# Optimization experiments

Measured on AMD Instinct MI355X. Metric: run time of the kernel, lower is better.

## Reference

```python
import jax, jax.numpy as jnp
import numpy as np

B, S, D, H, MEL = 64, 512, 512, 8, 80
HD = D // H  # head dim


def _lstm_cell(x, h, c, w_ih, w_hh, b_ih, b_hh):
    # torch gate order: i, f, g, o
    gates = x @ w_ih.T + h @ w_hh.T + b_ih + b_hh
    i, f, g, o = jnp.split(gates, 4, axis=-1)
    c = jax.nn.sigmoid(f) * c + jax.nn.sigmoid(i) * jnp.tanh(g)
    h = jax.nn.sigmoid(o) * jnp.tanh(c)
    return h, c


def setup_inputs() -> dict:
    key = jax.random.key(0)
    ks = jax.random.split(key, 24)
    s = 0.05
    inp = {"encoder_output": jax.random.normal(ks[0], (B, S, D), jnp.float32)}
    # MultiheadAttention params (torch layout: in_proj [3D, D])
    inp["attn_in_w"] = jax.random.normal(ks[1], (3 * D, D), jnp.float32) * s
    inp["attn_in_b"] = jax.random.normal(ks[2], (3 * D,), jnp.float32) * s
    inp["attn_out_w"] = jax.random.normal(ks[3], (D, D), jnp.float32) * s
    inp["attn_out_b"] = jax.random.normal(ks[4], (D,), jnp.float32) * s
    # LSTM1 (2 layers)
    names = [("l1_w_ih0", (4 * D, D)), ("l1_w_hh0", (4 * D, D)), ("l1_b_ih0", (4 * D,)), ("l1_b_hh0", (4 * D,)),
             ("l1_w_ih1", (4 * D, D)), ("l1_w_hh1", (4 * D, D)), ("l1_b_ih1", (4 * D,)), ("l1_b_hh1", (4 * D,)),
             ("l2_w_ih", (4 * D, D)), ("l2_w_hh", (4 * D, D)), ("l2_b_ih", (4 * D,)), ("l2_b_hh", (4 * D,)),
             ("proj_w", (MEL, D)), ("proj_b", (MEL,))]
    for i, (n, shp) in enumerate(names):
        inp[n] = jax.random.normal(ks[5 + i], shp, jnp.float32) * s
    return inp


def reference(encoder_output, attn_in_w, attn_in_b, attn_out_w, attn_out_b,
              l1_w_ih0, l1_w_hh0, l1_b_ih0, l1_b_hh0,
              l1_w_ih1, l1_w_hh1, l1_b_ih1, l1_b_hh1,
              l2_w_ih, l2_w_hh, l2_b_ih, l2_b_hh, proj_w, proj_b):
    b, s, d = encoder_output.shape
    max_len = s * 5
    wq, wk, wv = jnp.split(attn_in_w, 3, axis=0)
    bq, bk, bv = jnp.split(attn_in_b, 3, axis=0)
    # Precompute K, V over encoder output: [B, S, H, HD]
    K = (encoder_output @ wk.T + bk).reshape(b, s, H, HD)
    V = (encoder_output @ wv.T + bv).reshape(b, s, H, HD)
    scale = 1.0 / np.sqrt(HD)

    def attend(x):  # x: [B, D] single-token query
        q = ((x @ wq.T + bq) * scale).reshape(b, H, HD)
        scores = jnp.einsum('bhd,bshd->bhs', q, K)
        w = jax.nn.softmax(scores, axis=-1)
        ctx = jnp.einsum('bhs,bshd->bhd', w, V).reshape(b, d)
        return ctx @ attn_out_w.T + attn_out_b

    zeros = jnp.zeros((b, d), encoder_output.dtype)
    carry0 = (zeros, zeros, zeros, zeros, zeros, zeros, zeros)

    def step(carry, _):
        h10, c10, h11, c11, h2, c2, dec_in = carry
        h10, c10 = _lstm_cell(dec_in, h10, c10, l1_w_ih0, l1_w_hh0, l1_b_ih0, l1_b_hh0)
        h11, c11 = _lstm_cell(h10, h11, c11, l1_w_ih1, l1_w_hh1, l1_b_ih1, l1_b_hh1)
        attn_out = attend(h11)
        h2, c2 = _lstm_cell(attn_out, h2, c2, l2_w_ih, l2_w_hh, l2_b_ih, l2_b_hh)
        out = h2 @ proj_w.T + proj_b  # [B, MEL]
        return (h10, c10, h11, c11, h2, c2, h2), out

    _, ys = jax.lax.scan(step, carry0, None, length=max_len)
    return jnp.transpose(ys, (1, 0, 2))  # [B, max_len, MEL]
```

## Files before the change

### kernel.cpp

```cpp
#include <hip/hip_runtime.h>
#include <hip/hip_bf16.h>
#include <hip/hip_fp8.h>

#define DEV_INLINE __device__ __forceinline__

typedef __attribute__((ext_vector_type(8))) short bf16x8;
typedef __attribute__((ext_vector_type(4))) float f32x4;
typedef unsigned long long ull;

constexpr int Bc = 64, Sc = 512, Dc = 512, Hc = 8, HDc = 64, MELc = 80, Tc = 2560;
constexpr int OUTSTRIDE = Tc * MELc;

constexpr size_t SZ_KP8 = 64ull * 8 * 512 * 64;
constexpr size_t SZ_VP  = 64ull * 8 * 512 * 64 * 2;
constexpr size_t SZ_PL  = 128ull * 2048 * 16;
constexpr size_t OFF_KP8 = 0;
constexpr size_t OFF_VP  = OFF_KP8 + SZ_KP8;
constexpr size_t OFF_PL0 = OFF_VP + SZ_VP;
constexpr size_t OFF_PL1 = OFF_PL0 + SZ_PL;
constexpr size_t OFF_PL2 = OFF_PL1 + SZ_PL;
constexpr size_t OFF_PWQ = OFF_PL2 + SZ_PL;
constexpr size_t OFF_PP  = OFF_PWQ + 524288;
constexpr size_t OFF_BL0 = OFF_PP + 81920;
constexpr size_t OFF_BL1 = OFF_BL0 + 8192;
constexpr size_t OFF_BL2 = OFF_BL1 + 8192;
constexpr size_t OFF_B2E = OFF_BL2 + 8192;
constexpr size_t OFF_W2E = OFF_B2E + 8192;
constexpr size_t OFF_WOT = OFF_W2E + 2097152;
constexpr size_t OFF_ACT = OFF_WOT + 1048576;
constexpr size_t OFF_FLG = OFF_ACT + 524288;

constexpr unsigned DYN_LDS = 137344;

DEV_INLINE float bf2f(short s) { return __uint_as_float(((unsigned)(unsigned short)s) << 16); }
DEV_INLINE short f2bf(float f) { union { __hip_bfloat16 h; short s; } u; u.h = __float2bfloat16(f); return u.s; }
DEV_INLINE float sig_f(float x) { return 1.0f / (1.0f + __expf(-x)); }
DEV_INLINE float tanh_f(float x) {
  float ax = fabsf(x);
  float e = __expf(fminf(2.0f * ax, 80.0f));
  float r = 1.0f - 2.0f / (e + 1.0f);
  return copysignf(r, x);
}
DEV_INLINE bf16x8 cvt8(const float* p) {
  bf16x8 r;
#pragma unroll
  for (int i = 0; i < 8; ++i) r[i] = f2bf(p[i]);
  return r;
}
DEV_INLINE float fp8tof(unsigned v) {
  __hip_fp8_e4m3 t; t.__x = (__hip_fp8_storage_t)v; return (float)t;
}

DEV_INLINE ull ld_dev_u64(const void* p) {
  return __hip_atomic_load((const ull*)p, __ATOMIC_RELAXED, __HIP_MEMORY_SCOPE_AGENT);
}
DEV_INLINE void st_dev_u64(void* p, ull v) {
  __hip_atomic_store((ull*)p, v, __ATOMIC_RELAXED, __HIP_MEMORY_SCOPE_AGENT);
}
DEV_INLINE bf16x8 ld_frag(const __hip_bfloat16* p) {
  union { bf16x8 v; ull u[2]; } r;
  r.u[0] = ld_dev_u64(p);
  r.u[1] = ld_dev_u64((const char*)p + 8);
  return r.v;
}

__global__ __launch_bounds__(256) void gemm_setup(const float* __restrict__ A,
                                                  const float* __restrict__ Bt,
                                                  const float* __restrict__ bias,
                                                  __hip_bfloat16* __restrict__ dst,
                                                  unsigned char* __restrict__ dst8,
                                                  int mode) {
  int tid = threadIdx.x, lane = tid & 63, wv = tid >> 6;
  int m0 = blockIdx.y * 64 + wv * 16;
  int nb = blockIdx.x * 64;
  int mrow = m0 + (lane & 15);
  int kb = (lane >> 4) * 8;
  f32x4 acc0 = {0,0,0,0}, acc1 = {0,0,0,0}, acc2 = {0,0,0,0}, acc3 = {0,0,0,0};
  const float* arow = A + (size_t)mrow * 512 + kb;
  const float* b0r = Bt + (size_t)(nb + 0 * 16 + (lane & 15)) * 512 + kb;
  const float* b1r = Bt + (size_t)(nb + 1 * 16 + (lane & 15)) * 512 + kb;
  const float* b2r = Bt + (size_t)(nb + 2 * 16 + (lane & 15)) * 512 + kb;
  const float* b3r = Bt + (size_t)(nb + 3 * 16 + (lane & 15)) * 512 + kb;
  for (int kk = 0; kk < 16; ++kk) {
    bf16x8 af = cvt8(arow + kk * 32);
    acc0 = __builtin_amdgcn_mfma_f32_16x16x32_bf16(af, cvt8(b0r + kk * 32), acc0, 0, 0, 0);
    acc1 = __builtin_amdgcn_mfma_f32_16x16x32_bf16(af, cvt8(b1r + kk * 32), acc1, 0, 0, 0);
    acc2 = __builtin_amdgcn_mfma_f32_16x16x32_bf16(af, cvt8(b2r + kk * 32), acc2, 0, 0, 0);
    acc3 = __builtin_amdgcn_mfma_f32_16x16x32_bf16(af, cvt8(b3r + kk * 32), acc3, 0, 0, 0);
  }
  int col16 = lane & 15, r0 = (lane >> 4) * 4;
  f32x4 accs[4] = {acc0, acc1, acc2, acc3};
#pragma unroll
  for (int nt = 0; nt < 4; ++nt) {
    int n = nb + nt * 16 + col16;
#pragma unroll
    for (int r = 0; r < 4; ++r) {
      int m = m0 + r0 + r;
      float v = accs[nt][r];
      if (mode == 0) {
        v += bias[n];
        int bb = m >> 9, s = m & 511, h = n >> 6, d = n & 63;
        dst[(((size_t)(bb * 8 + h) * 512 + s) * 64) + d] = __float2bfloat16(v);
      } else if (mode == 2) {
        v += bias[n];
        int bb = m >> 9, s = m & 511, h = n >> 6, d = n & 63;
        __hip_fp8_e4m3 q(v);
        dst8[(((size_t)(bb * 8 + h) * 512 + s) * 64) + d] = (unsigned char)q.__x;
      } else {
        dst[(size_t)m * 512 + n] = __float2bfloat16(v);
      }
    }
  }
}

__global__ __launch_bounds__(256) void transpose512(const float* __restrict__ in, float* __restrict__ out) {
  __shared__ float tl[32][33];
  int x = threadIdx.x & 31, ty = threadIdx.x >> 5;
  int bx = blockIdx.x * 32, by = blockIdx.y * 32;
#pragma unroll
  for (int r = 0; r < 4; ++r) tl[ty + r * 8][x] = in[(size_t)(by + ty + r * 8) * 512 + bx + x];
  __syncthreads();
#pragma unroll
  for (int r = 0; r < 4; ++r) out[(size_t)(bx + ty + r * 8) * 512 + by + x] = tl[x][ty + r * 8];
}

__global__ __launch_bounds__(256) void b2eff_k(const float* __restrict__ w2ih, const float* __restrict__ bout,
                                               const float* __restrict__ bih, const float* __restrict__ bhh,
                                               float* __restrict__ dst) {
  int g = blockIdx.x * 256 + threadIdx.x;
  float acc = bih[g] + bhh[g];
  const float* row = w2ih + (size_t)g * 512;
  for (int k = 0; k < 512; ++k) acc += row[k] * bout[k];
  dst[g] = acc;
}

__global__ __launch_bounds__(256) void pack_lstm(const float* __restrict__ lo_f32,
                                                 const __hip_bfloat16* __restrict__ lo_bf16,
                                                 const float* __restrict__ hi_f32,
                                                 const float* __restrict__ b1, const float* __restrict__ b2,
                                                 const float* __restrict__ b_pre,
                                                 __hip_bfloat16* __restrict__ dst, float* __restrict__ bias_out,
                                                 int mode) {
  int u = blockIdx.x, tid = threadIdx.x;
  for (int rep = 0; rep < 8; ++rep) {
    int slot = rep * 256 + tid;
    int kk = slot >> 6, lane = slot & 63;
    int n16 = lane & 15, gate = n16 >> 2, jj = n16 & 3;
    int srow = gate * 512 + u * 4 + jj;
    int k = kk * 32 + (lane >> 4) * 8;
    __hip_bfloat16 tmp[8];
    if (k < 512) {
      if (mode == 0) {
#pragma unroll
        for (int i = 0; i < 8; ++i) tmp[i] = __float2bfloat16(lo_f32[(size_t)srow * 512 + k + i]);
      } else {
#pragma unroll
        for (int i = 0; i < 8; ++i) tmp[i] = lo_bf16[(size_t)srow * 512 + k + i];
      }
    } else {
#pragma unroll
      for (int i = 0; i < 8; ++i) tmp[i] = __float2bfloat16(hi_f32[(size_t)srow * 512 + (k - 512) + i]);
    }
    *(uint4*)(dst + ((size_t)u * 2048 + slot) * 8) = *(uint4*)tmp;
  }
  if (tid < 16) {
    int gate = tid >> 2, jj = tid & 3;
    int srow = gate * 512 + u * 4 + jj;
    bias_out[u * 16 + tid] = (mode == 0) ? (b1[srow] + b2[srow]) : b_pre[srow];
  }
}

__global__ __launch_bounds__(256) void pack_wq(const float* __restrict__ wq, __hip_bfloat16* __restrict__ dst) {
  int h = blockIdx.x, tid = threadIdx.x;
  for (int rep = 0; rep < 16; ++rep) {
    int slot = rep * 256 + tid;
    int nt = slot >> 10, kk = (slot >> 6) & 15, lane = slot & 63;
    int srow = h * 64 + nt * 16 + (lane & 15);
    int k = kk * 32 + (lane >> 4) * 8;
    __hip_bfloat16 tmp[8];
#pragma unroll
    for (int i = 0; i < 8; ++i) tmp[i] = __float2bfloat16(wq[(size_t)srow * 512 + k + i]);
    *(uint4*)(dst + ((size_t)h * 4096 + slot) * 8) = *(uint4*)tmp;
  }
}

__global__ __launch_bounds__(256) void pack_proj(const float* __restrict__ pw, __hip_bfloat16* __restrict__ dst) {
  int u5 = blockIdx.x, tid = threadIdx.x;
  for (int rep = 0; rep < 4; ++rep) {
    int slot = rep * 256 + tid;
    int kk = slot >> 6, lane = slot & 63;
    int srow = u5 * 16 + (lane & 15);
    int k = kk * 32 + (lane >> 4) * 8;
    __hip_bfloat16 tmp[8];
#pragma unroll
    for (int i = 0; i < 8; ++i) tmp[i] = __float2bfloat16(pw[(size_t)srow * 512 + k + i]);
    *(uint4*)(dst + ((size_t)u5 * 1024 + slot) * 8) = *(uint4*)tmp;
  }
}

struct DecParams {
  const float* attn_in_b;
  const float* proj_b;
  const uint4* packL0; const uint4* packL1; const uint4* packL2;
  const float* biasL0; const float* biasL1; const float* biasL2;
  const uint4* packWq; const uint4* packP;
  const unsigned char* Kp8; const __hip_bfloat16* Vp;
  __hip_bfloat16* h10b; __hip_bfloat16* h11b; __hip_bfloat16* h2b; __hip_bfloat16* ctxb;
  ull* actbase;
  unsigned* flags;
  float* out;
};

constexpr ull WD_TICKS = 200000000ull;

DEV_INLINE void publish_flag(unsigned* flags, int wg, unsigned id, int tid) {
  __builtin_amdgcn_s_waitcnt(0);
  __syncthreads();
  if (tid == 0)
    __hip_atomic_store(&flags[wg], id, __ATOMIC_RELAXED, __HIP_MEMORY_SCOPE_AGENT);
}

DEV_INLINE bool wait_flags(unsigned* flags, int base, int count, unsigned id, int tid,
                           ull t0, int* bail) {
  if (tid < 64) {
    for (;;) {
      bool ok = true;
      for (int i = tid; i < count; i += 64)
        ok &= (__hip_atomic_load(&flags[base + i], __ATOMIC_RELAXED, __HIP_MEMORY_SCOPE_AGENT) >= id);
      if (__all(ok ? 1 : 0)) break;
      if (__builtin_amdgcn_s_memrealtime() - t0 > WD_TICKS) { if (tid == 0) *bail = 1; break; }
      __builtin_amdgcn_s_sleep(1);
    }
  }
  __syncthreads();
  if (*bail) return false;
  return true;
}

DEV_INLINE void prefetch_hi(bf16x8* pf, const __hip_bfloat16* hi, int g, int lane, int wv) {
  if (wv >= 2) {
    const __hip_bfloat16* p = hi + (size_t)(g * 32 + (wv & 1) * 16 + (lane & 15)) * 512 + (lane >> 4) * 8;
#pragma unroll
    for (int kk = 0; kk < 16; ++kk) pf[kk] = ld_frag(p + kk * 32);
  }
}

DEV_INLINE void lstm_stage(int tid, int g, int wgl,
                           const uint4* wlds, const float* bias,
                           const __hip_bfloat16* lo, const bf16x8* pf,
                           float* cstate, __hip_bfloat16* hc,
                           float* pred, ull* st64) {
  const int lane = tid & 63, wv = tid >> 6, mt = wv & 1, kh = wv >> 1;
  f32x4 acc = {0,0,0,0};
  if (kh == 0) {
    const __hip_bfloat16* pA = lo + (size_t)(g * 32 + mt * 16 + (lane & 15)) * 512 + (lane >> 4) * 8;
#pragma unroll
    for (int kk = 0; kk < 16; ++kk) {
      bf16x8 a = ld_frag(pA + kk * 32);
      bf16x8 b = *(const bf16x8*)(wlds + kk * 64 + lane);
      acc = __builtin_amdgcn_mfma_f32_16x16x32_bf16(a, b, acc, 0, 0, 0);
    }
  } else {
#pragma unroll
    for (int kk = 0; kk < 16; ++kk) {
      bf16x8 b = *(const bf16x8*)(wlds + (16 + kk) * 64 + lane);
      acc = __builtin_amdgcn_mfma_f32_16x16x32_bf16(pf[kk], b, acc, 0, 0, 0);
    }
  }
#pragma unroll
  for (int r = 0; r < 4; ++r) pred[wv * 256 + lane * 4 + r] = acc[r];
  __syncthreads();
  if (tid < 128) {
    int bl = tid >> 2, j = tid & 3;
    int mt2 = bl >> 4, qd = (bl & 15) >> 2, reg = bl & 3;
    const float* p0 = pred + mt2 * 256;
    const float* p1 = pred + (2 + mt2) * 256;
    int l0 = qd * 16;
    float gi = p0[(l0 + j) * 4 + reg]      + p1[(l0 + j) * 4 + reg]      + bias[j];
    float gf = p0[(l0 + 4 + j) * 4 + reg]  + p1[(l0 + 4 + j) * 4 + reg]  + bias[4 + j];
    float gg = p0[(l0 + 8 + j) * 4 + reg]  + p1[(l0 + 8 + j) * 4 + reg]  + bias[8 + j];
    float go = p0[(l0 + 12 + j) * 4 + reg] + p1[(l0 + 12 + j) * 4 + reg] + bias[12 + j];
    float c = cstate[tid & 127];
    c = sig_f(gf) * c + sig_f(gi) * tanh_f(gg);
    float h = sig_f(go) * tanh_f(c);
    cstate[tid & 127] = c;
    ((unsigned short*)st64)[tid] = (unsigned short)f2bf(h);
  }
  __syncthreads();
  if (tid < 32)
    st_dev_u64(hc + (size_t)(g * 32 + tid) * 512 + wgl * 4, st64[tid]);
}

DEV_INLINE void proj_stage(int tid, int g, int n5, const uint4* wPJ, const float* proj_b,
                           const __hip_bfloat16* h2in, float* outp, float* pred) {
  const int lane = tid & 63, wv = tid >> 6, mt = wv & 1, kh = wv >> 1;
  f32x4 acc = {0,0,0,0};
  const __hip_bfloat16* pA = h2in + (size_t)(g * 32 + mt * 16 + (lane & 15)) * 512 + kh * 256 + (lane >> 4) * 8;
#pragma unroll
  for (int kk = 0; kk < 8; ++kk) {
    bf16x8 a = ld_frag(pA + kk * 32);
    bf16x8 b = *(const bf16x8*)(wPJ + (kh * 8 + kk) * 64 + lane);
    acc = __builtin_amdgcn_mfma_f32_16x16x32_bf16(a, b, acc, 0, 0, 0);
  }
#pragma unroll
  for (int r = 0; r < 4; ++r) pred[wv * 256 + lane * 4 + r] = acc[r];
  __syncthreads();
#pragma unroll
  for (int half = 0; half < 2; ++half) {
    int gx = half * 256 + tid;
    int row = gx >> 4, col = gx & 15;
    int mt2 = row >> 4, qd = (row & 15) >> 2, reg = row & 3, ln = qd * 16 + col;
    float v = pred[mt2 * 256 + ln * 4 + reg] + pred[(2 + mt2) * 256 + ln * 4 + reg] + proj_b[n5 * 16 + col];
    outp[(size_t)(g * 32 + row) * OUTSTRIDE + n5 * 16 + col] = v;
  }
  __syncthreads();
}

__global__ __launch_bounds__(256, 1) void decoder_main(DecParams P) {
  extern __shared__ char smem[];
  uint4* wL0 = (uint4*)smem;
  uint4* wL1 = wL0 + 2048;
  uint4* wL2 = wL1 + 2048;
  uint4* wPJ = wL2 + 2048;
  ull*   st64 = (ull*)(wPJ + 1024);
  float* pred = (float*)(st64 + 32);
  float* qls  = pred + 1024;
  float* sco  = qls + 1088;
  float* red  = sco + 1024;
  float* cst  = red + 2048;
  float* smx  = cst + 384;
  float* ssum = smx + 4;
  float* sinv = ssum + 4;
  int*   sbail = (int*)(sinv + 2);

  const int wg = blockIdx.x, tid = threadIdx.x;
  const int lane = tid & 63, wv = tid >> 6;
  const int g = wg >> 7;
  const int wgl = wg & 127;
  const int fbase = g * 128;
  const int hh = wgl >> 4;
  const int b0g = (wgl & 15) * 2;
  const int bblk = b0g & ~15;

  const ull t0 = __builtin_amdgcn_s_memrealtime();

  {
    const uint4* s0 = P.packL0 + (size_t)wgl * 2048;
    const uint4* s1 = P.packL1 + (size_t)wgl * 2048;
    const uint4* s2 = P.packL2 + (size_t)wgl * 2048;
    for (int i = tid; i < 2048; i += 256) { wL0[i] = s0[i]; wL1[i] = s1[i]; wL2[i] = s2[i]; }
    if (wgl < 5) { const uint4* sp = P.packP + (size_t)wgl * 1024; for (int i = tid; i < 1024; i += 256) wPJ[i] = sp[i]; }
  }
  if (tid == 0) *sbail = 0;
  if (tid < 128) { cst[tid] = 0.0f; cst[128 + tid] = 0.0f; cst[256 + tid] = 0.0f; }
  st_dev_u64(P.actbase + (size_t)wg * 256 + tid, 0ull);
  __syncthreads();
  publish_flag(P.flags, wg, 1u, tid);
  if (!wait_flags(P.flags, 0, 256, 1u, tid, t0, sbail)) goto bail;

  for (int t = 0; t < Tc; ++t) {
    const int cur = t & 1, pv = cur ^ 1;
    const unsigned idA = 4u * t + 1, idApub = 4u * t + 2, idBpub = 4u * t + 3,
                   idCpub = 4u * t + 4, idDpub = 4u * t + 5;
    __hip_bfloat16* h10c = P.h10b + cur * 32768; __hip_bfloat16* h10p = P.h10b + pv * 32768;
    __hip_bfloat16* h11c = P.h11b + cur * 32768; __hip_bfloat16* h11p = P.h11b + pv * 32768;
    __hip_bfloat16* h2c  = P.h2b  + cur * 32768; __hip_bfloat16* h2p  = P.h2b  + pv * 32768;
    __hip_bfloat16* ctxc = P.ctxb + cur * 32768;

    {
      bf16x8 pf[16];
      prefetch_hi(pf, h10p, g, lane, wv);
      if (!wait_flags(P.flags, fbase, 128, idA, tid, t0, sbail)) goto bail;
      lstm_stage(tid, g, wgl, wL0, P.biasL0 + wgl * 16, h2p, pf, cst, h10c, pred, st64);
      publish_flag(P.flags, wg, idApub, tid);
    }
    if (wgl < 5 && t > 0)
      proj_stage(tid, g, wgl, wPJ, P.proj_b, h2p, P.out + (size_t)(t - 1) * MELc, pred);

    {
      bf16x8 pf[16];
      prefetch_hi(pf, h11p, g, lane, wv);
      if (!wait_flags(P.flags, fbase, 128, idApub, tid, t0, sbail)) goto bail;
      lstm_stage(tid, g, wgl, wL1, P.biasL1 + wgl * 16, h10c, pf, cst + 128, h11c, pred, st64);
      publish_flag(P.flags, wg, idBpub, tid);
    }

    if (!wait_flags(P.flags, fbase, 128, idBpub, tid, t0, sbail)) goto bail;
    {
      int mrow = g * 32 + bblk + (lane & 15);
      const __hip_bfloat16* pA = h11c + (size_t)mrow * 512 + (lane >> 4) * 8;
      const uint4* pB = P.packWq + (size_t)hh * 4096 + wv * 1024;
      f32x4 acc = {0,0,0,0};
#pragma unroll
      for (int kk = 0; kk < 16; ++kk) {
        bf16x8 a = ld_frag(pA + kk * 32);
        bf16x8 b = *(const bf16x8*)(pB + kk * 64 + lane);
        acc = __builtin_amdgcn_mfma_f32_16x16x32_bf16(a, b, acc, 0, 0, 0);
      }
      int col = lane & 15, row0 = (lane >> 4) << 2;
      int dg = wv * 16 + col;
      float bq = P.attn_in_b[hh * 64 + dg];
#pragma unroll
      for (int r = 0; r < 4; ++r) qls[(row0 + r) * 68 + dg] = (acc[r] + bq) * 0.125f;
    }
    __syncthreads();
    {
      int p = tid >> 7, si = tid & 127;
      int bg = g * 32 + b0g + p;
      const float* qv = qls + ((b0g & 15) + p) * 68;
      const ull* Kb = (const ull*)(P.Kp8 + (size_t)(bg * 8 + hh) * 512 * 64);
#pragma unroll
      for (int ss = 0; ss < 4; ++ss) {
        int s = si * 4 + ss;
        const ull* kr = Kb + (size_t)s * 8;
        float acc = 0.0f;
#pragma unroll
        for (int i = 0; i < 8; ++i) {
          ull kv = kr[i];
#pragma unroll
          for (int jj = 0; jj < 8; ++jj)
            acc += qv[i * 8 + jj] * fp8tof((unsigned)(kv >> (8 * jj)) & 0xFFu);
        }
        sco[p * 512 + s] = acc;
      }
    }
    __syncthreads();
    {
      int p = wv >> 1, half = wv & 1;
      int idx = tid & 127;
      float mx = -1e30f;
#pragma unroll
      for (int ss = 0; ss < 4; ++ss) mx = fmaxf(mx, sco[p * 512 + idx * 4 + ss]);
#pragma unroll
      for (int off = 32; off; off >>= 1) mx = fmaxf(mx, __shfl_xor(mx, off));
      if (lane == 0) smx[p * 2 + half] = mx;
      __syncthreads();
      float m = fmaxf(smx[p * 2], smx[p * 2 + 1]);
      float sum = 0.0f;
#pragma unroll
      for (int ss = 0; ss < 4; ++ss) {
        int ix = p * 512 + idx * 4 + ss;
        float e = __expf(sco[ix] - m);
        sco[ix] = e; sum += e;
      }
#pragma unroll
      for (int off = 32; off; off >>= 1) sum += __shfl_xor(sum, off);
      if (lane == 0) ssum[p * 2 + half] = sum;
      __syncthreads();
      if (tid < 2) sinv[tid] = 1.0f / (ssum[tid * 2] + ssum[tid * 2 + 1]);
    }
    __syncthreads();
    {
      int p = wv >> 1, half = wv & 1;
      int bg = g * 32 + b0g + p;
      int sg = lane >> 3, dj = lane & 7;
      const __hip_bfloat16* Vb = P.Vp + (size_t)(bg * 8 + hh) * 512 * 64;
      float a8[8] = {0,0,0,0,0,0,0,0};
      for (int it = 0; it < 32; ++it) {
        int s = half * 256 + it * 8 + sg;
        float w = sco[p * 512 + s];
        bf16x8 v = *(const bf16x8*)(Vb + (size_t)s * 64 + dj * 8);
#pragma unroll
        for (int e = 0; e < 8; ++e) a8[e] += w * bf2f(v[e]);
      }
      float* rp = red + ((p * 16 + half * 8 + sg) * 64) + dj * 8;
#pragma unroll
      for (int e = 0; e < 8; ++e) rp[e] = a8[e];
    }
    __syncthreads();
    if (tid < 128) {
      int p = tid >> 6, d = tid & 63;
      float sacc = 0.0f;
#pragma unroll
      for (int k = 0; k < 16; ++k) sacc += red[(p * 16 + k) * 64 + d];
      sacc *= sinv[p];
      ((unsigned short*)st64)[tid] = (unsigned short)f2bf(sacc);
    }
    __syncthreads();
    if (tid < 32) {
      int p = tid >> 4, q = tid & 15;
      st_dev_u64(ctxc + (size_t)(g * 32 + b0g + p) * 512 + hh * 64 + q * 4, st64[p * 16 + q]);
    }
    publish_flag(P.flags, wg, idCpub, tid);

    {
      bf16x8 pf[16];
      prefetch_hi(pf, h2p, g, lane, wv);
      if (!wait_flags(P.flags, fbase, 128, idCpub, tid, t0, sbail)) goto bail;
      lstm_stage(tid, g, wgl, wL2, P.biasL2 + wgl * 16, ctxc, pf, cst + 256, h2c, pred, st64);
      publish_flag(P.flags, wg, idDpub, tid);
    }
  }

  if (wgl < 5) {
    if (wait_flags(P.flags, fbase, 128, 4u * (Tc - 1) + 5, tid, t0, sbail))
      proj_stage(tid, g, wgl, wPJ, P.proj_b, P.h2b + ((Tc - 1) & 1) * 32768,
                 P.out + (size_t)(Tc - 1) * MELc, pred);
  }
  return;

bail:
  publish_flag(P.flags, wg, 0x7F000000u, tid);
}

extern "C" void kernel_launch(void* const* d_in, const int* in_sizes, int n_in,
                              void* d_out, int out_size, void* d_ws, size_t ws_size,
                              hipStream_t stream) {
  const float* enc        = (const float*)d_in[0];
  const float* attn_in_w  = (const float*)d_in[1];
  const float* attn_in_b  = (const float*)d_in[2];
  const float* attn_out_w = (const float*)d_in[3];
  const float* attn_out_b = (const float*)d_in[4];
  const float* w_ih0 = (const float*)d_in[5];
  const float* w_hh0 = (const float*)d_in[6];
  const float* b_ih0 = (const float*)d_in[7];
  const float* b_hh0 = (const float*)d_in[8];
  const float* w_ih1 = (const float*)d_in[9];
  const float* w_hh1 = (const float*)d_in[10];
  const float* b_ih1 = (const float*)d_in[11];
  const float* b_hh1 = (const float*)d_in[12];
  const float* w_ih2 = (const float*)d_in[13];
  const float* w_hh2 = (const float*)d_in[14];
  const float* b_ih2 = (const float*)d_in[15];
  const float* b_hh2 = (const float*)d_in[16];
  const float* proj_w = (const float*)d_in[17];
  const float* proj_b = (const float*)d_in[18];

  char* ws = (char*)d_ws;
  unsigned char*  Kp8 = (unsigned char*)(ws + OFF_KP8);
  __hip_bfloat16* Vp  = (__hip_bfloat16*)(ws + OFF_VP);
  __hip_bfloat16* pl0 = (__hip_bfloat16*)(ws + OFF_PL0);
  __hip_bfloat16* pl1 = (__hip_bfloat16*)(ws + OFF_PL1);
  __hip_bfloat16* pl2 = (__hip_bfloat16*)(ws + OFF_PL2);
  __hip_bfloat16* pwq = (__hip_bfloat16*)(ws + OFF_PWQ);
  __hip_bfloat16* pp  = (__hip_bfloat16*)(ws + OFF_PP);
  float* bl0 = (float*)(ws + OFF_BL0);
  float* bl1 = (float*)(ws + OFF_BL1);
  float* bl2 = (float*)(ws + OFF_BL2);
  float* b2e = (float*)(ws + OFF_B2E);
  __hip_bfloat16* w2e = (__hip_bfloat16*)(ws + OFF_W2E);
  float* wot = (float*)(ws + OFF_WOT);
  char* act  = ws + OFF_ACT;
  unsigned* flags = (unsigned*)(ws + OFF_FLG);

  hipMemsetAsync(flags, 0, 4096, stream);

  gemm_setup<<<dim3(8, 512), 256, 0, stream>>>(enc, attn_in_w + 512 * 512, attn_in_b + 512, nullptr, Kp8, 2);
  gemm_setup<<<dim3(8, 512), 256, 0, stream>>>(enc, attn_in_w + 1024 * 512, attn_in_b + 1024, Vp, nullptr, 0);
  transpose512<<<dim3(16, 16), 256, 0, stream>>>(attn_out_w, wot);
  gemm_setup<<<dim3(8, 32), 256, 0, stream>>>(w_ih2, wot, nullptr, w2e, nullptr, 1);
  b2eff_k<<<8, 256, 0, stream>>>(w_ih2, attn_out_b, b_ih2, b_hh2, b2e);
  pack_lstm<<<128, 256, 0, stream>>>(w_ih0, nullptr, w_hh0, b_ih0, b_hh0, nullptr, pl0, bl0, 0);
  pack_lstm<<<128, 256, 0, stream>>>(w_ih1, nullptr, w_hh1, b_ih1, b_hh1, nullptr, pl1, bl1, 0);
  pack_lstm<<<128, 256, 0, stream>>>(nullptr, w2e, w_hh2, nullptr, nullptr, b2e, pl2, bl2, 1);
  pack_wq<<<8, 256, 0, stream>>>(attn_in_w, pwq);
  pack_proj<<<5, 256, 0, stream>>>(proj_w, pp);

  DecParams p;
  p.attn_in_b = attn_in_b;
  p.proj_b = proj_b;
  p.packL0 = (const uint4*)pl0; p.packL1 = (const uint4*)pl1; p.packL2 = (const uint4*)pl2;
  p.biasL0 = bl0; p.biasL1 = bl1; p.biasL2 = bl2;
  p.packWq = (const uint4*)pwq; p.packP = (const uint4*)pp;
  p.Kp8 = Kp8; p.Vp = Vp;
  p.h10b = (__hip_bfloat16*)(act + 0);
  p.h11b = (__hip_bfloat16*)(act + 131072);
  p.h2b  = (__hip_bfloat16*)(act + 262144);
  p.ctxb = (__hip_bfloat16*)(act + 393216);
  p.actbase = (ull*)act;
  p.flags = flags;
  p.out = (float*)d_out;

  (void)hipFuncSetAttribute((const void*)decoder_main,
                            hipFuncAttributeMaxDynamicSharedMemorySize, DYN_LDS);
  decoder_main<<<dim3(256), dim3(256), DYN_LDS, stream>>>(p);
}
```

Baseline: 110.9 ms.

## Keep per-workgroup K/V resident in LDS as FP8, stream LSTM weights from global

Swaps which data lives in LDS for the persistent decoder. K (fp8) and V, now quantized to fp8 instead of bf16, for each workgroup's two batch-head slices are loaded once into LDS with padded K rows. The LSTM and projection weight packs, which used to sit in LDS, are now read from global memory every step. This removes per-step global reads of K/V in attention, at the cost of extra global/L2 traffic for weights, fp8 precision loss on V, and a larger LDS footprint.

```diff
diff --git a/kernel.cpp b/kernel.cpp
--- a/kernel.cpp
+++ b/kernel.cpp
@@ -12,11 +12,11 @@
 constexpr int OUTSTRIDE = Tc * MELc;
 
 constexpr size_t SZ_KP8 = 64ull * 8 * 512 * 64;
-constexpr size_t SZ_VP  = 64ull * 8 * 512 * 64 * 2;
+constexpr size_t SZ_VP8 = 64ull * 8 * 512 * 64;
 constexpr size_t SZ_PL  = 128ull * 2048 * 16;
 constexpr size_t OFF_KP8 = 0;
-constexpr size_t OFF_VP  = OFF_KP8 + SZ_KP8;
-constexpr size_t OFF_PL0 = OFF_VP + SZ_VP;
+constexpr size_t OFF_VP8 = OFF_KP8 + SZ_KP8;
+constexpr size_t OFF_PL0 = OFF_VP8 + SZ_VP8;
 constexpr size_t OFF_PL1 = OFF_PL0 + SZ_PL;
 constexpr size_t OFF_PL2 = OFF_PL1 + SZ_PL;
 constexpr size_t OFF_PWQ = OFF_PL2 + SZ_PL;
@@ -30,7 +30,16 @@
 constexpr size_t OFF_ACT = OFF_WOT + 1048576;
 constexpr size_t OFF_FLG = OFF_ACT + 524288;
 
-constexpr unsigned DYN_LDS = 137344;
+constexpr unsigned LDS_KK   = 0;
+constexpr unsigned LDS_KV   = 69632;
+constexpr unsigned LDS_PRED = 135168;
+constexpr unsigned LDS_QLS  = 139264;
+constexpr unsigned LDS_SCO  = 143616;
+constexpr unsigned LDS_RED  = 147712;
+constexpr unsigned LDS_CST  = 155904;
+constexpr unsigned LDS_ST64 = 157440;
+constexpr unsigned LDS_MISC = 157696;
+constexpr unsigned DYN_LDS  = 157760;
 
 DEV_INLINE float bf2f(short s) { return __uint_as_float(((unsigned)(unsigned short)s) << 16); }
 DEV_INLINE short f2bf(float f) { union { __hip_bfloat16 h; short s; } u; u.h = __float2bfloat16(f); return u.s; }
@@ -97,11 +106,7 @@
     for (int r = 0; r < 4; ++r) {
       int m = m0 + r0 + r;
       float v = accs[nt][r];
-      if (mode == 0) {
-        v += bias[n];
-        int bb = m >> 9, s = m & 511, h = n >> 6, d = n & 63;
-        dst[(((size_t)(bb * 8 + h) * 512 + s) * 64) + d] = __float2bfloat16(v);
-      } else if (mode == 2) {
+      if (mode == 2) {
         v += bias[n];
         int bb = m >> 9, s = m & 511, h = n >> 6, d = n & 63;
         __hip_fp8_e4m3 q(v);
@@ -204,7 +209,7 @@
   const uint4* packL0; const uint4* packL1; const uint4* packL2;
   const float* biasL0; const float* biasL1; const float* biasL2;
   const uint4* packWq; const uint4* packP;
-  const unsigned char* Kp8; const __hip_bfloat16* Vp;
+  const unsigned char* Kp8; const unsigned char* Vp8;
   __hip_bfloat16* h10b; __hip_bfloat16* h11b; __hip_bfloat16* h2b; __hip_bfloat16* ctxb;
   ull* actbase;
   unsigned* flags;
@@ -246,7 +251,7 @@
 }
 
 DEV_INLINE void lstm_stage(int tid, int g, int wgl,
-                           const uint4* wlds, const float* bias,
+                           const uint4* packW, const float* bias,
                            const __hip_bfloat16* lo, const bf16x8* pf,
                            float* cstate, __hip_bfloat16* hc,
                            float* pred, ull* st64) {
@@ -257,13 +262,13 @@
 #pragma unroll
     for (int kk = 0; kk < 16; ++kk) {
       bf16x8 a = ld_frag(pA + kk * 32);
-      bf16x8 b = *(const bf16x8*)(wlds + kk * 64 + lane);
+      bf16x8 b = *(const bf16x8*)(packW + kk * 64 + lane);
       acc = __builtin_amdgcn_mfma_f32_16x16x32_bf16(a, b, acc, 0, 0, 0);
     }
   } else {
 #pragma unroll
     for (int kk = 0; kk < 16; ++kk) {
-      bf16x8 b = *(const bf16x8*)(wlds + (16 + kk) * 64 + lane);
+      bf16x8 b = *(const bf16x8*)(packW + (16 + kk) * 64 + lane);
       acc = __builtin_amdgcn_mfma_f32_16x16x32_bf16(pf[kk], b, acc, 0, 0, 0);
     }
   }
@@ -318,17 +323,15 @@
 
 __global__ __launch_bounds__(256, 1) void decoder_main(DecParams P) {
   extern __shared__ char smem[];
-  uint4* wL0 = (uint4*)smem;
-  uint4* wL1 = wL0 + 2048;
-  uint4* wL2 = wL1 + 2048;
-  uint4* wPJ = wL2 + 2048;
-  ull*   st64 = (ull*)(wPJ + 1024);
-  float* pred = (float*)(st64 + 32);
-  float* qls  = pred + 1024;
-  float* sco  = qls + 1088;
-  float* red  = sco + 1024;
-  float* cst  = red + 2048;
-  float* smx  = cst + 384;
+  char* kK   = smem + LDS_KK;
+  char* kV   = smem + LDS_KV;
+  float* pred = (float*)(smem + LDS_PRED);
+  float* qls  = (float*)(smem + LDS_QLS);
+  float* sco  = (float*)(smem + LDS_SCO);
+  float* red  = (float*)(smem + LDS_RED);
+  float* cst  = (float*)(smem + LDS_CST);
+  ull*   st64 = (ull*)(smem + LDS_ST64);
+  float* smx  = (float*)(smem + LDS_MISC);
   float* ssum = smx + 4;
   float* sinv = ssum + 4;
   int*   sbail = (int*)(sinv + 2);
@@ -343,14 +346,29 @@
   const int bblk = b0g & ~15;
 
   const ull t0 = __builtin_amdgcn_s_memrealtime();
-
-  {
-    const uint4* s0 = P.packL0 + (size_t)wgl * 2048;
-    const uint4* s1 = P.packL1 + (size_t)wgl * 2048;
-    const uint4* s2 = P.packL2 + (size_t)wgl * 2048;
-    for (int i = tid; i < 2048; i += 256) { wL0[i] = s0[i]; wL1[i] = s1[i]; wL2[i] = s2[i]; }
-    if (wgl < 5) { const uint4* sp = P.packP + (size_t)wgl * 1024; for (int i = tid; i < 1024; i += 256) wPJ[i] = sp[i]; }
-  }
+  const uint4* myL0 = P.packL0 + (size_t)wgl * 2048;
+  const uint4* myL1 = P.packL1 + (size_t)wgl * 2048;
+  const uint4* myL2 = P.packL2 + (size_t)wgl * 2048;
+
+#pragma unroll
+  for (int pr = 0; pr < 2; ++pr) {
+    int bg = g * 32 + b0g + pr;
+    const unsigned char* srcK = P.Kp8 + (size_t)(bg * 8 + hh) * 512 * 64;
+    const ull* srcV = (const ull*)(P.Vp8 + (size_t)(bg * 8 + hh) * 512 * 64);
+    for (int r = 0; r < 2; ++r) {
+      int s = r * 256 + tid;
+      const uint4* g4 = (const uint4*)(srcK + (size_t)s * 64);
+      uint4 q0 = g4[0], q1 = g4[1], q2 = g4[2], q3 = g4[3];
+      unsigned* dp = (unsigned*)(kK + pr * 34816 + s * 68);
+      dp[0] = q0.x; dp[1] = q0.y; dp[2] = q0.z; dp[3] = q0.w;
+      dp[4] = q1.x; dp[5] = q1.y; dp[6] = q1.z; dp[7] = q1.w;
+      dp[8] = q2.x; dp[9] = q2.y; dp[10] = q2.z; dp[11] = q2.w;
+      dp[12] = q3.x; dp[13] = q3.y; dp[14] = q3.z; dp[15] = q3.w;
+    }
+    ull* dv = (ull*)(kV + pr * 32768);
+    for (int i = tid; i < 4096; i += 256) dv[i] = srcV[i];
+  }
+
   if (tid == 0) *sbail = 0;
   if (tid < 128) { cst[tid] = 0.0f; cst[128 + tid] = 0.0f; cst[256 + tid] = 0.0f; }
   st_dev_u64(P.actbase + (size_t)wg * 256 + tid, 0ull);
@@ -371,17 +389,18 @@
       bf16x8 pf[16];
       prefetch_hi(pf, h10p, g, lane, wv);
       if (!wait_flags(P.flags, fbase, 128, idA, tid, t0, sbail)) goto bail;
-      lstm_stage(tid, g, wgl, wL0, P.biasL0 + wgl * 16, h2p, pf, cst, h10c, pred, st64);
+      lstm_stage(tid, g, wgl, myL0, P.biasL0 + wgl * 16, h2p, pf, cst, h10c, pred, st64);
       publish_flag(P.flags, wg, idApub, tid);
     }
     if (wgl < 5 && t > 0)
-      proj_stage(tid, g, wgl, wPJ, P.proj_b, h2p, P.out + (size_t)(t - 1) * MELc, pred);
+      proj_stage(tid, g, wgl, P.packP + (size_t)wgl * 1024, P.proj_b, h2p,
+                 P.out + (size_t)(t - 1) * MELc, pred);
 
     {
       bf16x8 pf[16];
       prefetch_hi(pf, h11p, g, lane, wv);
       if (!wait_flags(P.flags, fbase, 128, idApub, tid, t0, sbail)) goto bail;
-      lstm_stage(tid, g, wgl, wL1, P.biasL1 + wgl * 16, h10c, pf, cst + 128, h11c, pred, st64);
+      lstm_stage(tid, g, wgl, myL1, P.biasL1 + wgl * 16, h10c, pf, cst + 128, h11c, pred, st64);
       publish_flag(P.flags, wg, idBpub, tid);
     }
 
@@ -406,20 +425,20 @@
     __syncthreads();
     {
       int p = tid >> 7, si = tid & 127;
-      int bg = g * 32 + b0g + p;
       const float* qv = qls + ((b0g & 15) + p) * 68;
-      const ull* Kb = (const ull*)(P.Kp8 + (size_t)(bg * 8 + hh) * 512 * 64);
+      const char* Kb = kK + p * 34816;
 #pragma unroll
       for (int ss = 0; ss < 4; ++ss) {
-        int s = si * 4 + ss;
-        const ull* kr = Kb + (size_t)s * 8;
+        int s = ss * 128 + si;
+        const unsigned* kr = (const unsigned*)(Kb + s * 68);
         float acc = 0.0f;
 #pragma unroll
-        for (int i = 0; i < 8; ++i) {
-          ull kv = kr[i];
-#pragma unroll
-          for (int jj = 0; jj < 8; ++jj)
-            acc += qv[i * 8 + jj] * fp8tof((unsigned)(kv >> (8 * jj)) & 0xFFu);
+        for (int i = 0; i < 16; ++i) {
+          unsigned kv = kr[i];
+          acc += qv[i * 4 + 0] * fp8tof(kv & 0xFFu);
+          acc += qv[i * 4 + 1] * fp8tof((kv >> 8) & 0xFFu);
+          acc += qv[i * 4 + 2] * fp8tof((kv >> 16) & 0xFFu);
+          acc += qv[i * 4 + 3] * fp8tof(kv >> 24);
         }
         sco[p * 512 + s] = acc;
       }
@@ -452,16 +471,15 @@
     __syncthreads();
     {
       int p = wv >> 1, half = wv & 1;
-      int bg = g * 32 + b0g + p;
       int sg = lane >> 3, dj = lane & 7;
-      const __hip_bfloat16* Vb = P.Vp + (size_t)(bg * 8 + hh) * 512 * 64;
+      const char* Vb = kV + p * 32768;
       float a8[8] = {0,0,0,0,0,0,0,0};
       for (int it = 0; it < 32; ++it) {
         int s = half * 256 + it * 8 + sg;
         float w = sco[p * 512 + s];
-        bf16x8 v = *(const bf16x8*)(Vb + (size_t)s * 64 + dj * 8);
-#pragma unroll
-        for (int e = 0; e < 8; ++e) a8[e] += w * bf2f(v[e]);
+        ull v = *(const ull*)(Vb + s * 64 + dj * 8);
+#pragma unroll
+        for (int e = 0; e < 8; ++e) a8[e] += w * fp8tof((unsigned)(v >> (8 * e)) & 0xFFu);
       }
       float* rp = red + ((p * 16 + half * 8 + sg) * 64) + dj * 8;
 #pragma unroll
@@ -487,15 +505,15 @@
       bf16x8 pf[16];
       prefetch_hi(pf, h2p, g, lane, wv);
       if (!wait_flags(P.flags, fbase, 128, idCpub, tid, t0, sbail)) goto bail;
-      lstm_stage(tid, g, wgl, wL2, P.biasL2 + wgl * 16, ctxc, pf, cst + 256, h2c, pred, st64);
+      lstm_stage(tid, g, wgl, myL2, P.biasL2 + wgl * 16, ctxc, pf, cst + 256, h2c, pred, st64);
       publish_flag(P.flags, wg, idDpub, tid);
     }
   }
 
   if (wgl < 5) {
     if (wait_flags(P.flags, fbase, 128, 4u * (Tc - 1) + 5, tid, t0, sbail))
-      proj_stage(tid, g, wgl, wPJ, P.proj_b, P.h2b + ((Tc - 1) & 1) * 32768,
-                 P.out + (size_t)(Tc - 1) * MELc, pred);
+      proj_stage(tid, g, wgl, P.packP + (size_t)wgl * 1024, P.proj_b,
+                 P.h2b + ((Tc - 1) & 1) * 32768, P.out + (size_t)(Tc - 1) * MELc, pred);
   }
   return;
 
@@ -528,7 +546,7 @@
 
   char* ws = (char*)d_ws;
   unsigned char*  Kp8 = (unsigned char*)(ws + OFF_KP8);
-  __hip_bfloat16* Vp  = (__hip_bfloat16*)(ws + OFF_VP);
+  unsigned char*  Vp8 = (unsigned char*)(ws + OFF_VP8);
   __hip_bfloat16* pl0 = (__hip_bfloat16*)(ws + OFF_PL0);
   __hip_bfloat16* pl1 = (__hip_bfloat16*)(ws + OFF_PL1);
   __hip_bfloat16* pl2 = (__hip_bfloat16*)(ws + OFF_PL2);
@@ -546,7 +564,7 @@
   hipMemsetAsync(flags, 0, 4096, stream);
 
   gemm_setup<<<dim3(8, 512), 256, 0, stream>>>(enc, attn_in_w + 512 * 512, attn_in_b + 512, nullptr, Kp8, 2);
-  gemm_setup<<<dim3(8, 512), 256, 0, stream>>>(enc, attn_in_w + 1024 * 512, attn_in_b + 1024, Vp, nullptr, 0);
+  gemm_setup<<<dim3(8, 512), 256, 0, stream>>>(enc, attn_in_w + 1024 * 512, attn_in_b + 1024, nullptr, Vp8, 2);
   transpose512<<<dim3(16, 16), 256, 0, stream>>>(attn_out_w, wot);
   gemm_setup<<<dim3(8, 32), 256, 0, stream>>>(w_ih2, wot, nullptr, w2e, nullptr, 1);
   b2eff_k<<<8, 256, 0, stream>>>(w_ih2, attn_out_b, b_ih2, b_hh2, b2e);
@@ -562,7 +580,7 @@
   p.packL0 = (const uint4*)pl0; p.packL1 = (const uint4*)pl1; p.packL2 = (const uint4*)pl2;
   p.biasL0 = bl0; p.biasL1 = bl1; p.biasL2 = bl2;
   p.packWq = (const uint4*)pwq; p.packP = (const uint4*)pp;
-  p.Kp8 = Kp8; p.Vp = Vp;
+  p.Kp8 = Kp8; p.Vp8 = Vp8;
   p.h10b = (__hip_bfloat16*)(act + 0);
   p.h11b = (__hip_bfloat16*)(act + 131072);
   p.h2b  = (__hip_bfloat16*)(act + 262144);
```

Result: slower. 145.1 ms (+30.9%).

## Replace per-workgroup flag polling with atomic counters and store V in fp8

Applied to the files above, without the earlier changes.

Inter-workgroup synchronization switches from each workgroup publishing its own flag and 64 lanes polling 128 flags, to per-stage atomic counters (padded to separate cache lines) that one thread increments and one thread polls against a target. The V cache is also quantized to fp8 e4m3 instead of bf16, halving the bytes streamed in the attention context pass each step. Counter atomics may contend across 128 workgroups, and fp8 V lowers numerical precision of the context vectors. The LDS layout is rewritten with explicit offsets but keeps the same total size.

```diff
diff --git a/kernel.cpp b/kernel.cpp
--- a/kernel.cpp
+++ b/kernel.cpp
@@ -12,11 +12,11 @@
 constexpr int OUTSTRIDE = Tc * MELc;
 
 constexpr size_t SZ_KP8 = 64ull * 8 * 512 * 64;
-constexpr size_t SZ_VP  = 64ull * 8 * 512 * 64 * 2;
+constexpr size_t SZ_VP8 = 64ull * 8 * 512 * 64;
 constexpr size_t SZ_PL  = 128ull * 2048 * 16;
 constexpr size_t OFF_KP8 = 0;
-constexpr size_t OFF_VP  = OFF_KP8 + SZ_KP8;
-constexpr size_t OFF_PL0 = OFF_VP + SZ_VP;
+constexpr size_t OFF_VP8 = OFF_KP8 + SZ_KP8;
+constexpr size_t OFF_PL0 = OFF_VP8 + SZ_VP8;
 constexpr size_t OFF_PL1 = OFF_PL0 + SZ_PL;
 constexpr size_t OFF_PL2 = OFF_PL1 + SZ_PL;
 constexpr size_t OFF_PWQ = OFF_PL2 + SZ_PL;
@@ -28,9 +28,22 @@
 constexpr size_t OFF_W2E = OFF_B2E + 8192;
 constexpr size_t OFF_WOT = OFF_W2E + 2097152;
 constexpr size_t OFF_ACT = OFF_WOT + 1048576;
-constexpr size_t OFF_FLG = OFF_ACT + 524288;
-
-constexpr unsigned DYN_LDS = 137344;
+constexpr size_t OFF_CTR = OFF_ACT + 524288;
+
+constexpr unsigned LDS_WL0  = 0;
+constexpr unsigned LDS_WL1  = 32768;
+constexpr unsigned LDS_WL2  = 65536;
+constexpr unsigned LDS_WPJ  = 98304;
+constexpr unsigned LDS_PRED = 114688;
+constexpr unsigned LDS_QLS  = 118784;
+constexpr unsigned LDS_SCO  = 123136;
+constexpr unsigned LDS_RED  = 127232;
+constexpr unsigned LDS_CST  = 135424;
+constexpr unsigned LDS_ST64 = 136960;
+constexpr unsigned LDS_MISC = 137216;
+constexpr unsigned DYN_LDS  = 137344;
+
+DEV_INLINE unsigned* ctr_ptr(unsigned* base, int idx) { return base + idx * 32; }
 
 DEV_INLINE float bf2f(short s) { return __uint_as_float(((unsigned)(unsigned short)s) << 16); }
 DEV_INLINE short f2bf(float f) { union { __hip_bfloat16 h; short s; } u; u.h = __float2bfloat16(f); return u.s; }
@@ -97,11 +110,7 @@
     for (int r = 0; r < 4; ++r) {
       int m = m0 + r0 + r;
       float v = accs[nt][r];
-      if (mode == 0) {
-        v += bias[n];
-        int bb = m >> 9, s = m & 511, h = n >> 6, d = n & 63;
-        dst[(((size_t)(bb * 8 + h) * 512 + s) * 64) + d] = __float2bfloat16(v);
-      } else if (mode == 2) {
+      if (mode == 2) {
         v += bias[n];
         int bb = m >> 9, s = m & 511, h = n >> 6, d = n & 63;
         __hip_fp8_e4m3 q(v);
@@ -204,37 +213,32 @@
   const uint4* packL0; const uint4* packL1; const uint4* packL2;
   const float* biasL0; const float* biasL1; const float* biasL2;
   const uint4* packWq; const uint4* packP;
-  const unsigned char* Kp8; const __hip_bfloat16* Vp;
+  const unsigned char* Kp8; const unsigned char* Vp8;
   __hip_bfloat16* h10b; __hip_bfloat16* h11b; __hip_bfloat16* h2b; __hip_bfloat16* ctxb;
   ull* actbase;
-  unsigned* flags;
+  unsigned* ctrs;
   float* out;
 };
 
 constexpr ull WD_TICKS = 200000000ull;
 
-DEV_INLINE void publish_flag(unsigned* flags, int wg, unsigned id, int tid) {
+DEV_INLINE void publish_ctr(unsigned* c, int tid) {
   __builtin_amdgcn_s_waitcnt(0);
   __syncthreads();
   if (tid == 0)
-    __hip_atomic_store(&flags[wg], id, __ATOMIC_RELAXED, __HIP_MEMORY_SCOPE_AGENT);
-}
-
-DEV_INLINE bool wait_flags(unsigned* flags, int base, int count, unsigned id, int tid,
-                           ull t0, int* bail) {
-  if (tid < 64) {
-    for (;;) {
-      bool ok = true;
-      for (int i = tid; i < count; i += 64)
-        ok &= (__hip_atomic_load(&flags[base + i], __ATOMIC_RELAXED, __HIP_MEMORY_SCOPE_AGENT) >= id);
-      if (__all(ok ? 1 : 0)) break;
-      if (__builtin_amdgcn_s_memrealtime() - t0 > WD_TICKS) { if (tid == 0) *bail = 1; break; }
+    (void)__hip_atomic_fetch_add(c, 1u, __ATOMIC_RELAXED, __HIP_MEMORY_SCOPE_AGENT);
+}
+
+DEV_INLINE bool wait_ctr(const unsigned* c, unsigned target, int tid,
+                         ull t0, int* bail) {
+  if (tid == 0) {
+    while (__hip_atomic_load(c, __ATOMIC_RELAXED, __HIP_MEMORY_SCOPE_AGENT) < target) {
+      if (__builtin_amdgcn_s_memrealtime() - t0 > WD_TICKS) { *bail = 1; break; }
       __builtin_amdgcn_s_sleep(1);
     }
   }
   __syncthreads();
-  if (*bail) return false;
-  return true;
+  return !*bail;
 }
 
 DEV_INLINE void prefetch_hi(bf16x8* pf, const __hip_bfloat16* hi, int g, int lane, int wv) {
@@ -318,17 +322,17 @@
 
 __global__ __launch_bounds__(256, 1) void decoder_main(DecParams P) {
   extern __shared__ char smem[];
-  uint4* wL0 = (uint4*)smem;
-  uint4* wL1 = wL0 + 2048;
-  uint4* wL2 = wL1 + 2048;
-  uint4* wPJ = wL2 + 2048;
-  ull*   st64 = (ull*)(wPJ + 1024);
-  float* pred = (float*)(st64 + 32);
-  float* qls  = pred + 1024;
-  float* sco  = qls + 1088;
-  float* red  = sco + 1024;
-  float* cst  = red + 2048;
-  float* smx  = cst + 384;
+  uint4* wL0  = (uint4*)(smem + LDS_WL0);
+  uint4* wL1  = (uint4*)(smem + LDS_WL1);
+  uint4* wL2  = (uint4*)(smem + LDS_WL2);
+  uint4* wPJ  = (uint4*)(smem + LDS_WPJ);
+  float* pred = (float*)(smem + LDS_PRED);
+  float* qls  = (float*)(smem + LDS_QLS);
+  float* sco  = (float*)(smem + LDS_SCO);
+  float* red  = (float*)(smem + LDS_RED);
+  float* cst  = (float*)(smem + LDS_CST);
+  ull*   st64 = (ull*)(smem + LDS_ST64);
+  float* smx  = (float*)(smem + LDS_MISC);
   float* ssum = smx + 4;
   float* sinv = ssum + 4;
   int*   sbail = (int*)(sinv + 2);
@@ -337,12 +341,16 @@
   const int lane = tid & 63, wv = tid >> 6;
   const int g = wg >> 7;
   const int wgl = wg & 127;
-  const int fbase = g * 128;
   const int hh = wgl >> 4;
   const int b0g = (wgl & 15) * 2;
   const int bblk = b0g & ~15;
 
   const ull t0 = __builtin_amdgcn_s_memrealtime();
+  unsigned* cInit = ctr_ptr(P.ctrs, 0);
+  unsigned* cA = ctr_ptr(P.ctrs, 1 + g * 4 + 0);
+  unsigned* cB = ctr_ptr(P.ctrs, 1 + g * 4 + 1);
+  unsigned* cC = ctr_ptr(P.ctrs, 1 + g * 4 + 2);
+  unsigned* cD = ctr_ptr(P.ctrs, 1 + g * 4 + 3);
 
   {
     const uint4* s0 = P.packL0 + (size_t)wgl * 2048;
@@ -355,13 +363,12 @@
   if (tid < 128) { cst[tid] = 0.0f; cst[128 + tid] = 0.0f; cst[256 + tid] = 0.0f; }
   st_dev_u64(P.actbase + (size_t)wg * 256 + tid, 0ull);
   __syncthreads();
-  publish_flag(P.flags, wg, 1u, tid);
-  if (!wait_flags(P.flags, 0, 256, 1u, tid, t0, sbail)) goto bail;
+  publish_ctr(cInit, tid);
+  if (!wait_ctr(cInit, 256u, tid, t0, sbail)) goto bail;
 
   for (int t = 0; t < Tc; ++t) {
     const int cur = t & 1, pv = cur ^ 1;
-    const unsigned idA = 4u * t + 1, idApub = 4u * t + 2, idBpub = 4u * t + 3,
-                   idCpub = 4u * t + 4, idDpub = 4u * t + 5;
+    const unsigned stepN = 128u * (unsigned)(t + 1);
     __hip_bfloat16* h10c = P.h10b + cur * 32768; __hip_bfloat16* h10p = P.h10b + pv * 32768;
     __hip_bfloat16* h11c = P.h11b + cur * 32768; __hip_bfloat16* h11p = P.h11b + pv * 32768;
     __hip_bfloat16* h2c  = P.h2b  + cur * 32768; __hip_bfloat16* h2p  = P.h2b  + pv * 32768;
@@ -370,9 +377,9 @@
     {
       bf16x8 pf[16];
       prefetch_hi(pf, h10p, g, lane, wv);
-      if (!wait_flags(P.flags, fbase, 128, idA, tid, t0, sbail)) goto bail;
+      if (t > 0 && !wait_ctr(cD, stepN - 128u, tid, t0, sbail)) goto bail;
       lstm_stage(tid, g, wgl, wL0, P.biasL0 + wgl * 16, h2p, pf, cst, h10c, pred, st64);
-      publish_flag(P.flags, wg, idApub, tid);
+      publish_ctr(cA, tid);
     }
     if (wgl < 5 && t > 0)
       proj_stage(tid, g, wgl, wPJ, P.proj_b, h2p, P.out + (size_t)(t - 1) * MELc, pred);
@@ -380,12 +387,12 @@
     {
       bf16x8 pf[16];
       prefetch_hi(pf, h11p, g, lane, wv);
-      if (!wait_flags(P.flags, fbase, 128, idApub, tid, t0, sbail)) goto bail;
+      if (!wait_ctr(cA, stepN, tid, t0, sbail)) goto bail;
       lstm_stage(tid, g, wgl, wL1, P.biasL1 + wgl * 16, h10c, pf, cst + 128, h11c, pred, st64);
-      publish_flag(P.flags, wg, idBpub, tid);
-    }
-
-    if (!wait_flags(P.flags, fbase, 128, idBpub, tid, t0, sbail)) goto bail;
+      publish_ctr(cB, tid);
+    }
+
+    if (!wait_ctr(cB, stepN, tid, t0, sbail)) goto bail;
     {
       int mrow = g * 32 + bblk + (lane & 15);
       const __hip_bfloat16* pA = h11c + (size_t)mrow * 512 + (lane >> 4) * 8;
@@ -454,14 +461,14 @@
       int p = wv >> 1, half = wv & 1;
       int bg = g * 32 + b0g + p;
       int sg = lane >> 3, dj = lane & 7;
-      const __hip_bfloat16* Vb = P.Vp + (size_t)(bg * 8 + hh) * 512 * 64;
+      const unsigned char* Vb = P.Vp8 + (size_t)(bg * 8 + hh) * 512 * 64;
       float a8[8] = {0,0,0,0,0,0,0,0};
       for (int it = 0; it < 32; ++it) {
         int s = half * 256 + it * 8 + sg;
         float w = sco[p * 512 + s];
-        bf16x8 v = *(const bf16x8*)(Vb + (size_t)s * 64 + dj * 8);
-#pragma unroll
-        for (int e = 0; e < 8; ++e) a8[e] += w * bf2f(v[e]);
+        ull v = *(const ull*)(Vb + (size_t)s * 64 + dj * 8);
+#pragma unroll
+        for (int e = 0; e < 8; ++e) a8[e] += w * fp8tof((unsigned)(v >> (8 * e)) & 0xFFu);
       }
       float* rp = red + ((p * 16 + half * 8 + sg) * 64) + dj * 8;
 #pragma unroll
@@ -481,26 +488,29 @@
       int p = tid >> 4, q = tid & 15;
       st_dev_u64(ctxc + (size_t)(g * 32 + b0g + p) * 512 + hh * 64 + q * 4, st64[p * 16 + q]);
     }
-    publish_flag(P.flags, wg, idCpub, tid);
+    publish_ctr(cC, tid);
 
     {
       bf16x8 pf[16];
       prefetch_hi(pf, h2p, g, lane, wv);
-      if (!wait_flags(P.flags, fbase, 128, idCpub, tid, t0, sbail)) goto bail;
+      if (!wait_ctr(cC, stepN, tid, t0, sbail)) goto bail;
       lstm_stage(tid, g, wgl, wL2, P.biasL2 + wgl * 16, ctxc, pf, cst + 256, h2c, pred, st64);
-      publish_flag(P.flags, wg, idDpub, tid);
+      publish_ctr(cD, tid);
     }
   }
 
   if (wgl < 5) {
-    if (wait_flags(P.flags, fbase, 128, 4u * (Tc - 1) + 5, tid, t0, sbail))
+    if (wait_ctr(cD, 128u * (unsigned)Tc, tid, t0, sbail))
       proj_stage(tid, g, wgl, wPJ, P.proj_b, P.h2b + ((Tc - 1) & 1) * 32768,
                  P.out + (size_t)(Tc - 1) * MELc, pred);
   }
   return;
 
 bail:
-  publish_flag(P.flags, wg, 0x7F000000u, tid);
+  if (tid == 0)
+    for (int i = 0; i < 9; ++i)
+      (void)__hip_atomic_fetch_add(ctr_ptr(P.ctrs, i), 0x01000000u,
+                                   __ATOMIC_RELAXED, __HIP_MEMORY_SCOPE_AGENT);
 }
 
 extern "C" void kernel_launch(void* const* d_in, const int* in_sizes, int n_in,
@@ -528,7 +538,7 @@
 
   char* ws = (char*)d_ws;
   unsigned char*  Kp8 = (unsigned char*)(ws + OFF_KP8);
-  __hip_bfloat16* Vp  = (__hip_bfloat16*)(ws + OFF_VP);
+  unsigned char*  Vp8 = (unsigned char*)(ws + OFF_VP8);
   __hip_bfloat16* pl0 = (__hip_bfloat16*)(ws + OFF_PL0);
   __hip_bfloat16* pl1 = (__hip_bfloat16*)(ws + OFF_PL1);
   __hip_bfloat16* pl2 = (__hip_bfloat16*)(ws + OFF_PL2);
@@ -541,12 +551,12 @@
   __hip_bfloat16* w2e = (__hip_bfloat16*)(ws + OFF_W2E);
   float* wot = (float*)(ws + OFF_WOT);
   char* act  = ws + OFF_ACT;
-  unsigned* flags = (unsigned*)(ws + OFF_FLG);
-
-  hipMemsetAsync(flags, 0, 4096, stream);
+  unsigned* ctrs = (unsigned*)(ws + OFF_CTR);
+
+  hipMemsetAsync(ctrs, 0, 4096, stream);
 
   gemm_setup<<<dim3(8, 512), 256, 0, stream>>>(enc, attn_in_w + 512 * 512, attn_in_b + 512, nullptr, Kp8, 2);
-  gemm_setup<<<dim3(8, 512), 256, 0, stream>>>(enc, attn_in_w + 1024 * 512, attn_in_b + 1024, Vp, nullptr, 0);
+  gemm_setup<<<dim3(8, 512), 256, 0, stream>>>(enc, attn_in_w + 1024 * 512, attn_in_b + 1024, nullptr, Vp8, 2);
   transpose512<<<dim3(16, 16), 256, 0, stream>>>(attn_out_w, wot);
   gemm_setup<<<dim3(8, 32), 256, 0, stream>>>(w_ih2, wot, nullptr, w2e, nullptr, 1);
   b2eff_k<<<8, 256, 0, stream>>>(w_ih2, attn_out_b, b_ih2, b_hh2, b2e);
@@ -562,13 +572,13 @@
   p.packL0 = (const uint4*)pl0; p.packL1 = (const uint4*)pl1; p.packL2 = (const uint4*)pl2;
   p.biasL0 = bl0; p.biasL1 = bl1; p.biasL2 = bl2;
   p.packWq = (const uint4*)pwq; p.packP = (const uint4*)pp;
-  p.Kp8 = Kp8; p.Vp = Vp;
+  p.Kp8 = Kp8; p.Vp8 = Vp8;
   p.h10b = (__hip_bfloat16*)(act + 0);
   p.h11b = (__hip_bfloat16*)(act + 131072);
   p.h2b  = (__hip_bfloat16*)(act + 262144);
   p.ctxb = (__hip_bfloat16*)(act + 393216);
   p.actbase = (ull*)act;
-  p.flags = flags;
+  p.ctrs = ctrs;
   p.out = (float*)d_out;
 
   (void)hipFuncSetAttribute((const void*)decoder_main,
```

After: 115.8 ms. 4.5% more time.
